# Kernel optimization log

Hardware: AMD Instinct MI355X
Metric: run time of the kernel (lower is better)

## Reference

```python
import jax, jax.numpy as jnp
import numpy as np

N_NODES = 50000
N_EDGES = 600000
D_FEAT = 128


def setup_inputs() -> dict:
    key = jax.random.key(0)
    ks = jax.random.split(key, 10)
    x = jax.random.normal(ks[0], (N_NODES, D_FEAT), dtype=jnp.float32)
    src = jax.random.randint(ks[1], (N_EDGES,), 0, N_NODES, dtype=jnp.int32)
    dst = jax.random.randint(ks[2], (N_EDGES,), 0, N_NODES, dtype=jnp.int32)
    w1 = jax.random.normal(ks[3], (1, D_FEAT), dtype=jnp.float32) * 0.05
    Wd1 = jax.random.normal(ks[4], (D_FEAT, 64), dtype=jnp.float32) * 0.05
    b1 = jnp.zeros((64,), dtype=jnp.float32)
    w2 = jax.random.normal(ks[5], (1, 64), dtype=jnp.float32) * 0.05
    Wd2 = jax.random.normal(ks[6], (64, 32), dtype=jnp.float32) * 0.05
    b2 = jnp.zeros((32,), dtype=jnp.float32)
    Wout = jax.random.normal(ks[7], (32, 4), dtype=jnp.float32) * 0.05
    bout = jnp.zeros((4,), dtype=jnp.float32)
    return {"x": x, "src": src, "dst": dst, "w1": w1, "Wd1": Wd1, "b1": b1,
            "w2": w2, "Wd2": Wd2, "b2": b2, "Wout": Wout, "bout": bout}


def _spmm(src, dst, h):
    # A @ h for COO adjacency (edge src -> dst contributes h[src] into row dst)
    return jax.ops.segment_sum(h[src], dst, num_segments=N_NODES)


def reference(x, src, dst, w1, Wd1, b1, w2, Wd2, b2, Wout, bout):
    # input_layer is an Input wrapper: identity. Dropout is identity at inference.
    h = _spmm(src, dst, x) * w1          # GraphLayer 1: SpMM + elementwise scale
    h = h @ Wd1 + b1                     # Dense(64), linear activation
    h = _spmm(src, dst, h) * w2          # GraphLayer 2
    h = h @ Wd2 + b2                     # Dense(32)
    logits = h @ Wout + bout             # Dense(4)
    return jax.nn.softmax(logits, axis=-1)
```

## Files before the change

### kernel.cpp

```cpp
#include <hip/hip_runtime.h>
#include <hip/hip_bf16.h>

#define D_FEAT 128
#define NP 64
#define NP_SHIFT 6
#define P_PARTS 782
#define CAP 1024
#define EPB 2048


__global__ __launch_bounds__(256) void fused_xw_bucket_kernel(
    const float4* __restrict__ x4,
    const int* __restrict__ src,
    const int* __restrict__ dst,
    const float* __restrict__ w1,  const float* __restrict__ Wd1,
    const float* __restrict__ b1,  const float* __restrict__ w2,
    const float* __restrict__ Wd2, const float* __restrict__ b2,
    const float* __restrict__ Wout, const float* __restrict__ bout,
    int* __restrict__ partFill, int* __restrict__ edgeBuf,
    float* __restrict__ gc, float4* __restrict__ u4,
    int nN, int nE, int xwBlocks)
{
    __shared__ int sm[2 * P_PARTS];
    int t = threadIdx.x;

    if ((int)blockIdx.x < xwBlocks) {
        float* T2   = (float*)sm;
        float* Wall = (float*)sm + 256;
        {
            int m = t >> 2, j = t & 3;
            float s = 0.f;
            for (int p = 0; p < 32; ++p) s += Wd2[m * 32 + p] * Wout[p * 4 + j];
            T2[t] = w2[m] * s;
        }
        __syncthreads();
        for (int idx = t; idx < 512; idx += 256) {
            int k = idx >> 2, j = idx & 3;
            float s = 0.f;
            for (int m = 0; m < 64; ++m) s += Wd1[k * 64 + m] * T2[m * 4 + j];
            Wall[idx] = w1[k] * s;
        }
        if (blockIdx.x == 0 && t < 4) {
            float s = 0.f;
            for (int m = 0; m < 64; ++m) s += b1[m] * T2[m * 4 + t];
            gc[t] = s;
            float s2 = 0.f;
            for (int p = 0; p < 32; ++p) s2 += b2[p] * Wout[p * 4 + t];
            gc[4 + t] = s2 + bout[t];
        }
        __syncthreads();
        int r = blockIdx.x * 256 + t;
        if (r < nN) {
            const float4* W = (const float4*)Wall;
            float4 acc = make_float4(0.f, 0.f, 0.f, 0.f);
            #pragma unroll 8
            for (int k4 = 0; k4 < 32; ++k4) {
                float4 xv = x4[(size_t)r * 32 + k4];
                float4 w0 = W[4 * k4 + 0];
                float4 wv1 = W[4 * k4 + 1];
                float4 wv2 = W[4 * k4 + 2];
                float4 wv3 = W[4 * k4 + 3];
                acc.x += xv.x * w0.x + xv.y * wv1.x + xv.z * wv2.x + xv.w * wv3.x;
                acc.y += xv.x * w0.y + xv.y * wv1.y + xv.z * wv2.y + xv.w * wv3.y;
                acc.z += xv.x * w0.z + xv.y * wv1.z + xv.z * wv2.z + xv.w * wv3.z;
                acc.w += xv.x * w0.w + xv.y * wv1.w + xv.z * wv2.w + xv.w * wv3.w;
            }
            u4[r] = acc;
        }
    } else {
        int b = blockIdx.x - xwBlocks;
        int* hist = sm;
        int* base = sm + P_PARTS;
        for (int p = t; p < P_PARTS; p += 256) hist[p] = 0;
        __syncthreads();
        int beg = b * EPB + t;
        int end = min(b * EPB + EPB, nE);
        for (int i = beg; i < end; i += 256)
            atomicAdd(&hist[dst[i] >> NP_SHIFT], 1);
        __syncthreads();
        for (int p = t; p < P_PARTS; p += 256) {
            int h = hist[p];
            base[p] = h ? atomicAdd(&partFill[p], h) : 0;
        }
        __syncthreads();
        for (int i = beg; i < end; i += 256) {
            int d = dst[i];
            int p = d >> NP_SHIFT;
            int rank = atomicSub(&hist[p], 1) - 1;
            int pos = base[p] + rank;
            if (pos < CAP)
                edgeBuf[p * CAP + pos] = src[i] | ((d & (NP - 1)) << 16);
        }
    }
}

__global__ __launch_bounds__(256) void spmm_part_kernel(
    const int* __restrict__ partFill,
    const int* __restrict__ edgeBuf,
    const float4* __restrict__ in4,
    const float* __restrict__ gc, int gcOff,
    float4* __restrict__ out4, int nN, int doSoftmax)
{
    __shared__ float acc[NP * 4];
    int t = threadIdx.x, p = blockIdx.x;
    acc[t] = 0.f;
    __syncthreads();
    int n = min(partFill[p], CAP);
    const int* eb = edgeBuf + p * CAP;
    for (int i = t; i < n; i += 256) {
        int e = eb[i];
        float4 val = in4[e & 0xFFFF];
        int dl = e >> 16;
        atomicAdd(&acc[dl * 4 + 0], val.x);
        atomicAdd(&acc[dl * 4 + 1], val.y);
        atomicAdd(&acc[dl * 4 + 2], val.z);
        atomicAdd(&acc[dl * 4 + 3], val.w);
    }
    __syncthreads();
    if (t < NP) {
        int node = p * NP + t;
        if (node < nN) {
            float4 a = ((const float4*)acc)[t];
            float lx = a.x + gc[gcOff + 0];
            float ly = a.y + gc[gcOff + 1];
            float lz = a.z + gc[gcOff + 2];
            float lw = a.w + gc[gcOff + 3];
            if (doSoftmax) {
                float m = fmaxf(fmaxf(lx, ly), fmaxf(lz, lw));
                float ex = __expf(lx - m);
                float ey = __expf(ly - m);
                float ez = __expf(lz - m);
                float ew = __expf(lw - m);
                float r = 1.f / (ex + ey + ez + ew);
                out4[node] = make_float4(ex * r, ey * r, ez * r, ew * r);
            } else {
                out4[node] = make_float4(lx, ly, lz, lw);
            }
        }
    }
}

extern "C" void kernel_launch(void* const* d_in, const int* in_sizes, int n_in,
                              void* d_out, int out_size, void* d_ws, size_t ws_size,
                              hipStream_t stream)
{
    const float* x    = (const float*)d_in[0];
    const int*   src  = (const int*)d_in[1];
    const int*   dst  = (const int*)d_in[2];
    const float* w1   = (const float*)d_in[3];
    const float* Wd1  = (const float*)d_in[4];
    const float* b1   = (const float*)d_in[5];
    const float* w2   = (const float*)d_in[6];
    const float* Wd2  = (const float*)d_in[7];
    const float* b2   = (const float*)d_in[8];
    const float* Wout = (const float*)d_in[9];
    const float* bout = (const float*)d_in[10];

    const int nE = in_sizes[1];
    const int nN = in_sizes[0] / D_FEAT;

    float* ws = (float*)d_ws;
    float* gc = ws;
    float* u  = ws + 16;
    float* v  = u + (size_t)nN * 4;
    int* partFill = (int*)(v + (size_t)nN * 4);
    int* edgeBuf  = partFill + ((P_PARTS + 63) & ~63);

    const int xwBlocks = (nN + 255) / 256;
    const int bkBlocks = (nE + EPB - 1) / EPB;

    hipMemsetAsync(partFill, 0, P_PARTS * sizeof(int), stream);
    fused_xw_bucket_kernel<<<xwBlocks + bkBlocks, 256, 0, stream>>>(
        (const float4*)x, src, dst, w1, Wd1, b1, w2, Wd2, b2, Wout, bout,
        partFill, edgeBuf, gc, (float4*)u, nN, nE, xwBlocks);
    spmm_part_kernel<<<P_PARTS, 256, 0, stream>>>(partFill, edgeBuf,
                                                  (const float4*)u, gc, 0,
                                                  (float4*)v, nN, 0);
    spmm_part_kernel<<<P_PARTS, 256, 0, stream>>>(partFill, edgeBuf,
                                                  (const float4*)v, gc, 4,
                                                  (float4*)d_out, nN, 1);
}
```

Measured before the change: 143.9 us.

## Coalesce x projection loads, vectorize edge bucketing, and reshape SpMM accumulator layout

The x@W projection now assigns 8 lanes per row so that a wavefront reads contiguous float4s, keeps the weights in registers, and reduces the partial sums with shuffles. Edge bucketing reads src and dst as int4 with twice as many edges per block. The SpMM kernel loads each partition's edges as a single int4 per thread and stores the accumulator transposed and padded to spread shared-memory atomics across banks. The SpMM change assumes CAP equals 4 times the block size, so the old loop's generality is dropped.

```diff
diff --git a/kernel.cpp b/kernel.cpp
--- a/kernel.cpp
+++ b/kernel.cpp
@@ -1,12 +1,11 @@
 #include <hip/hip_runtime.h>
-#include <hip/hip_bf16.h>
 
 #define D_FEAT 128
 #define NP 64
 #define NP_SHIFT 6
 #define P_PARTS 782
 #define CAP 1024
-#define EPB 2048
+#define EPB 4096
 
 
 __global__ __launch_bounds__(256) void fused_xw_bucket_kernel(
@@ -21,12 +20,12 @@
     float* __restrict__ gc, float4* __restrict__ u4,
     int nN, int nE, int xwBlocks)
 {
-    __shared__ int sm[2 * P_PARTS];
+    __shared__ __align__(16) int sm[2 * P_PARTS];
     int t = threadIdx.x;
 
     if ((int)blockIdx.x < xwBlocks) {
-        float* T2   = (float*)sm;
-        float* Wall = (float*)sm + 256;
+        float*  T2 = (float*)sm;
+        float4* W4 = (float4*)(sm + 256);
         {
             int m = t >> 2, j = t & 3;
             float s = 0.f;
@@ -38,7 +37,7 @@
             int k = idx >> 2, j = idx & 3;
             float s = 0.f;
             for (int m = 0; m < 64; ++m) s += Wd1[k * 64 + m] * T2[m * 4 + j];
-            Wall[idx] = w1[k] * s;
+            ((float*)W4)[idx] = w1[k] * s;
         }
         if (blockIdx.x == 0 && t < 4) {
             float s = 0.f;
@@ -49,23 +48,42 @@
             gc[4 + t] = s2 + bout[t];
         }
         __syncthreads();
-        int r = blockIdx.x * 256 + t;
-        if (r < nN) {
-            const float4* W = (const float4*)Wall;
-            float4 acc = make_float4(0.f, 0.f, 0.f, 0.f);
-            #pragma unroll 8
-            for (int k4 = 0; k4 < 32; ++k4) {
-                float4 xv = x4[(size_t)r * 32 + k4];
-                float4 w0 = W[4 * k4 + 0];
-                float4 wv1 = W[4 * k4 + 1];
-                float4 wv2 = W[4 * k4 + 2];
-                float4 wv3 = W[4 * k4 + 3];
-                acc.x += xv.x * w0.x + xv.y * wv1.x + xv.z * wv2.x + xv.w * wv3.x;
-                acc.y += xv.x * w0.y + xv.y * wv1.y + xv.z * wv2.y + xv.w * wv3.y;
-                acc.z += xv.x * w0.z + xv.y * wv1.z + xv.z * wv2.z + xv.w * wv3.z;
-                acc.w += xv.x * w0.w + xv.y * wv1.w + xv.z * wv2.w + xv.w * wv3.w;
-            }
-            u4[r] = acc;
+
+        int lane = t & 63;
+        int li   = lane & 7;
+        int sub  = lane >> 3;
+        int wv   = t >> 6;
+        float4 wr[4][4];
+        #pragma unroll
+        for (int q = 0; q < 4; ++q)
+            #pragma unroll
+            for (int e = 0; e < 4; ++e)
+                wr[q][e] = W4[4 * (li + 8 * q) + e];
+
+        int R0 = blockIdx.x * 256;
+        #pragma unroll 2
+        for (int p = 0; p < 8; ++p) {
+            int r = R0 + p * 32 + wv * 8 + sub;
+            bool ok = r < nN;
+            size_t base = (size_t)r * 32 + li;
+            float4 a = make_float4(0.f, 0.f, 0.f, 0.f);
+            #pragma unroll
+            for (int q = 0; q < 4; ++q) {
+                float4 xv = ok ? x4[base + 8 * q]
+                               : make_float4(0.f, 0.f, 0.f, 0.f);
+                a.x += xv.x*wr[q][0].x + xv.y*wr[q][1].x + xv.z*wr[q][2].x + xv.w*wr[q][3].x;
+                a.y += xv.x*wr[q][0].y + xv.y*wr[q][1].y + xv.z*wr[q][2].y + xv.w*wr[q][3].y;
+                a.z += xv.x*wr[q][0].z + xv.y*wr[q][1].z + xv.z*wr[q][2].z + xv.w*wr[q][3].z;
+                a.w += xv.x*wr[q][0].w + xv.y*wr[q][1].w + xv.z*wr[q][2].w + xv.w*wr[q][3].w;
+            }
+            #pragma unroll
+            for (int m = 4; m >= 1; m >>= 1) {
+                a.x += __shfl_xor(a.x, m);
+                a.y += __shfl_xor(a.y, m);
+                a.z += __shfl_xor(a.z, m);
+                a.w += __shfl_xor(a.w, m);
+            }
+            if (ok && li == 0) u4[r] = a;
         }
     } else {
         int b = blockIdx.x - xwBlocks;
@@ -73,23 +91,50 @@
         int* base = sm + P_PARTS;
         for (int p = t; p < P_PARTS; p += 256) hist[p] = 0;
         __syncthreads();
-        int beg = b * EPB + t;
-        int end = min(b * EPB + EPB, nE);
-        for (int i = beg; i < end; i += 256)
-            atomicAdd(&hist[dst[i] >> NP_SHIFT], 1);
+        int beg = b * EPB;
+        int end = min(beg + EPB, nE);
+        for (int i4 = (beg >> 2) + t; i4 * 4 < end; i4 += 256) {
+            if (i4 * 4 + 3 < end) {
+                int4 d4 = ((const int4*)dst)[i4];
+                atomicAdd(&hist[d4.x >> NP_SHIFT], 1);
+                atomicAdd(&hist[d4.y >> NP_SHIFT], 1);
+                atomicAdd(&hist[d4.z >> NP_SHIFT], 1);
+                atomicAdd(&hist[d4.w >> NP_SHIFT], 1);
+            } else {
+                for (int i = i4 * 4; i < end; ++i)
+                    atomicAdd(&hist[dst[i] >> NP_SHIFT], 1);
+            }
+        }
         __syncthreads();
         for (int p = t; p < P_PARTS; p += 256) {
             int h = hist[p];
             base[p] = h ? atomicAdd(&partFill[p], h) : 0;
         }
         __syncthreads();
-        for (int i = beg; i < end; i += 256) {
-            int d = dst[i];
-            int p = d >> NP_SHIFT;
-            int rank = atomicSub(&hist[p], 1) - 1;
-            int pos = base[p] + rank;
-            if (pos < CAP)
-                edgeBuf[p * CAP + pos] = src[i] | ((d & (NP - 1)) << 16);
+        for (int i4 = (beg >> 2) + t; i4 * 4 < end; i4 += 256) {
+            if (i4 * 4 + 3 < end) {
+                int4 d4 = ((const int4*)dst)[i4];
+                int4 s4 = ((const int4*)src)[i4];
+                int dd[4] = {d4.x, d4.y, d4.z, d4.w};
+                int ss[4] = {s4.x, s4.y, s4.z, s4.w};
+                #pragma unroll
+                for (int j = 0; j < 4; ++j) {
+                    int p = dd[j] >> NP_SHIFT;
+                    int rank = atomicSub(&hist[p], 1) - 1;
+                    int pos = base[p] + rank;
+                    if (pos < CAP)
+                        edgeBuf[p * CAP + pos] = ss[j] | ((dd[j] & (NP - 1)) << 16);
+                }
+            } else {
+                for (int i = i4 * 4; i < end; ++i) {
+                    int d = dst[i];
+                    int p = d >> NP_SHIFT;
+                    int rank = atomicSub(&hist[p], 1) - 1;
+                    int pos = base[p] + rank;
+                    if (pos < CAP)
+                        edgeBuf[p * CAP + pos] = src[i] | ((d & (NP - 1)) << 16);
+                }
+            }
         }
     }
 }
@@ -101,30 +146,36 @@
     const float* __restrict__ gc, int gcOff,
     float4* __restrict__ out4, int nN, int doSoftmax)
 {
-    __shared__ float acc[NP * 4];
+    __shared__ float acc[4][72];
     int t = threadIdx.x, p = blockIdx.x;
-    acc[t] = 0.f;
+    for (int i = t; i < 288; i += 256) ((float*)acc)[i] = 0.f;
     __syncthreads();
     int n = min(partFill[p], CAP);
-    const int* eb = edgeBuf + p * CAP;
-    for (int i = t; i < n; i += 256) {
-        int e = eb[i];
-        float4 val = in4[e & 0xFFFF];
-        int dl = e >> 16;
-        atomicAdd(&acc[dl * 4 + 0], val.x);
-        atomicAdd(&acc[dl * 4 + 1], val.y);
-        atomicAdd(&acc[dl * 4 + 2], val.z);
-        atomicAdd(&acc[dl * 4 + 3], val.w);
+    int4 e4 = ((const int4*)(edgeBuf + p * CAP))[t];
+    int b0 = 4 * t;
+    {
+        int ee[4] = {e4.x, e4.y, e4.z, e4.w};
+        #pragma unroll
+        for (int j = 0; j < 4; ++j) {
+            if (b0 + j < n) {
+                int e = ee[j];
+                float4 val = in4[e & 0xFFFF];
+                int dl = e >> 16;
+                atomicAdd(&acc[0][dl], val.x);
+                atomicAdd(&acc[1][dl], val.y);
+                atomicAdd(&acc[2][dl], val.z);
+                atomicAdd(&acc[3][dl], val.w);
+            }
+        }
     }
     __syncthreads();
     if (t < NP) {
         int node = p * NP + t;
         if (node < nN) {
-            float4 a = ((const float4*)acc)[t];
-            float lx = a.x + gc[gcOff + 0];
-            float ly = a.y + gc[gcOff + 1];
-            float lz = a.z + gc[gcOff + 2];
-            float lw = a.w + gc[gcOff + 3];
+            float lx = acc[0][t] + gc[gcOff + 0];
+            float ly = acc[1][t] + gc[gcOff + 1];
+            float lz = acc[2][t] + gc[gcOff + 2];
+            float lw = acc[3][t] + gc[gcOff + 3];
             if (doSoftmax) {
                 float m = fmaxf(fmaxf(lx, ly), fmaxf(lz, lw));
                 float ex = __expf(lx - m);
```

New measurement: 150.8 us. +4.8%, slower.
